# Kernel optimization log

Hardware: AMD Instinct MI355X
Metric: run time of the kernel (lower is better)

## Reference

```python
import jax, jax.numpy as jnp
import numpy as np

B, CIN, COUT, H, W = 4, 4, 8, 256, 256
FFTH, FFTW = 2 * H - 1, 2 * W - 1  # fftsize = insize + outsize - 1 (padding=True, stride=1)


def setup_inputs() -> dict:
    key = jax.random.key(0)
    k_im, k_w, k_b = jax.random.split(key, 3)
    im = jax.random.normal(k_im, (B, CIN, H, W), dtype=jnp.float32)
    # learned frequency-domain kernel, last dim = (real, imag)
    weight = jax.random.normal(k_w, (COUT, CIN, FFTH, FFTW, 2), dtype=jnp.float32)
    bias = jax.random.normal(k_b, (COUT, 1, 1), dtype=jnp.float32)
    return {"im": im, "weight": weight, "bias": bias}


def reference(im, weight, bias):
    b, cin, h, w = im.shape
    ffth, fftw = 2 * h - 1, 2 * w - 1
    # zero-pad spatially to fftsize; imaginary part is zero (torch pads a trailing complex dim)
    im_p = jnp.pad(im, ((0, 0), (0, 0), (0, ffth - h), (0, fftw - w)))
    f_im = jnp.fft.fft2(im_p.astype(jnp.complex64))              # [B, Cin, fftH, fftW]
    wc = jax.lax.complex(weight[..., 0], weight[..., 1])         # [O, Cin, fftH, fftW]
    # broadcast complex multiply + in-channel reduction fused as a per-frequency contraction;
    # ifft is linear so summing over in-channels before ifft matches the original math
    feats = jnp.einsum('bchw,ochw->bohw', f_im, wc)              # [B, O, fftH, fftW]
    real = jnp.fft.ifft2(feats).real                             # real_feats_mode='index' -> real part
    # crop: cropsize = fftsize - insize = (H-1, W-1); left = floor/2, right = ceil/2
    cl_h, cr_h = (h - 1) // 2, h // 2
    cl_w, cr_w = (w - 1) // 2, w // 2
    real = real[:, :, cl_h:ffth - cr_h, cl_w:fftw - cr_w]        # [B, O, H, W]
    return real + bias                                           # bias [O,1,1] broadcasts
```

## Files before the change

kernel.cpp:

```cpp
#include <hip/hip_runtime.h>
#include <math.h>

#define NN 511
#define HH 256
#define BB 4
#define CINC 4
#define COUTC 8
#define CROP 127
#define INV_NN2 (1.0f / ((float)NN * (float)NN))

typedef _Float16 f16;
typedef _Float16 f16x8 __attribute__((ext_vector_type(8)));
typedef float    f32x4 __attribute__((ext_vector_type(4)));

__device__ __forceinline__ void twid(int a, int b, float& c, float& s) {
    int m = (int)(((long long)a * (long long)b) % NN);
    float phi = (float)(2.0 * M_PI / (double)NN) * (float)m;
    __sincosf(phi, &s, &c);
}

__global__ void prep_Aa(f16* __restrict__ Aa) {
    int idx = blockIdx.x * 256 + threadIdx.x;
    int m = idx >> 8, y = idx & 255;
    float c, s;
    if (m < 256) { twid(m, y, c, s);      Aa[idx] = (f16)c;    }
    else         { twid(m - 256, y, c, s); Aa[idx] = (f16)(-s); }
}
__global__ void prep_Bb(f16* __restrict__ Bb) {
    int idx = blockIdx.x * 256 + threadIdx.x;
    int n = idx >> 9, k = idx & 511;
    float v = 0.f;
    if (n < 2 * NN) {
        int vv = (n < NN) ? n : n - NN;
        int x  = k & 255;
        float c, s; twid(vv, x, c, s);
        if (n < NN) v = (k < 256) ? c : s;
        else        v = (k < 256) ? -s : c;
    }
    Bb[idx] = (f16)v;
}
__global__ void prep_Bd(f16* __restrict__ Bd) {
    int idx = blockIdx.x * 256 + threadIdx.x;
    int n = idx >> 10, k = idx & 1023;
    float v = 0.f;
    if (k < 2 * NN) {
        int x  = n & 255;
        int vv = (k < NN) ? k : k - NN;
        float c, s; twid(vv, x + CROP, c, s);
        if (n < 256) v = (k < NN) ? c : -s;
        else         v = (k < NN) ? s : c;
    }
    Bd[idx] = (f16)v;
}
__global__ void prep_Ae(f16* __restrict__ Ae) {
    int idx = blockIdx.x * 256 + threadIdx.x;
    int y = idx >> 9, k = idx & 511;
    float c, s;
    if (k < 256) { twid(k, y + CROP, c, s);       Ae[idx] = (f16)c;    }
    else         { twid(k - 256, y + CROP, c, s); Ae[idx] = (f16)(-s); }
}
__global__ void prep_imT(const float* __restrict__ im, f16* __restrict__ imT) {
    int idx = blockIdx.x * 256 + threadIdx.x;
    int bc = idx >> 16, r = idx & 65535;
    int y = r >> 8, x = r & 255;
    imT[(size_t)bc * 65536 + x * 256 + y] = (f16)im[idx];
}
__global__ void zero_pad1024(f16* __restrict__ buf, int rows) {
    int r = blockIdx.x * 256 + threadIdx.x;
    if (r < rows) {
        buf[(size_t)r * 1024 + 1022] = (f16)0.f;
        buf[(size_t)r * 1024 + 1023] = (f16)0.f;
    }
}

__global__ void cmul_h(const f16* __restrict__ F, const float2* __restrict__ W,
                       f16* __restrict__ feats) {
    int idx = blockIdx.x * 256 + threadIdx.x;
    if (idx >= 256 * NN) return;
    int u = idx / NN, v = idx - u * NN;
    int u2 = (u == 0) ? 0 : NN - u;
    int v2 = (v == 0) ? 0 : NN - v;
    float fr[BB][CINC], fi[BB][CINC];
    #pragma unroll
    for (int b = 0; b < BB; ++b)
        #pragma unroll
        for (int c = 0; c < CINC; ++c) {
            size_t row = ((size_t)((b * CINC + c) * 256 + u)) * 1024;
            fr[b][c] = (float)F[row + v];
            fi[b][c] = (float)F[row + NN + v];
        }
    #pragma unroll
    for (int o = 0; o < COUTC; ++o) {
        float whr[CINC], whi[CINC];
        #pragma unroll
        for (int c = 0; c < CINC; ++c) {
            size_t base = (size_t)(o * CINC + c) * NN;
            float2 w1 = W[(base + u)  * NN + v];
            float2 w2 = W[(base + u2) * NN + v2];
            whr[c] = 0.5f * (w1.x + w2.x);
            whi[c] = 0.5f * (w1.y - w2.y);
        }
        #pragma unroll
        for (int b = 0; b < BB; ++b) {
            float hr = 0.f, hi = 0.f;
            #pragma unroll
            for (int c = 0; c < CINC; ++c) {
                hr += fr[b][c] * whr[c] - fi[b][c] * whi[c];
                hi += fr[b][c] * whi[c] + fi[b][c] * whr[c];
            }
            size_t orow = ((size_t)((b * COUTC + o) * 256 + u)) * 1024;
            feats[orow + v]      = (f16)hr;
            feats[orow + NN + v] = (f16)hi;
        }
    }
}

#define GLB_PTR(p) ((const __attribute__((address_space(1))) unsigned int*)(p))
#define LDS_PTR(p) ((__attribute__((address_space(3))) unsigned int*)(p))
__device__ __forceinline__ void gld16(const f16* g, f16* l) {
    __builtin_amdgcn_global_load_lds(GLB_PTR(g), LDS_PTR(l), 16, 0, 0);
}

template<int EPI>
__global__ __launch_bounds__(256)
void gemm128x64(const f16* __restrict__ A, const f16* __restrict__ Bt,
                f16* __restrict__ Ch, float* __restrict__ Cf,
                const float* __restrict__ bias,
                int Kt, int ldA, int ldB, size_t sA, size_t sB) {
    __shared__ __align__(16) f16 As[128 * 32];
    __shared__ __align__(16) f16 Bs[64 * 32];

    const int z  = blockIdx.z;
    const int m0 = blockIdx.x * 128;
    const int n0 = blockIdx.y * 64;
    A  += (size_t)z * sA;
    Bt += (size_t)z * sB;

    const int t  = threadIdx.x;
    const int r4 = t >> 2;
    const int c8 = (t & 3) << 3;
    const f16* Ap = A  + (size_t)(m0 + r4) * ldA + c8;
    const f16* Bp = Bt + (size_t)(n0 + r4) * ldB + c8;
    f16* lA = As + t * 8;
    f16* lB = Bs + t * 8;

    const int lane = t & 63, w = t >> 6;
    const int wm = (w >> 1) * 64, wn = (w & 1) * 32;
    const int col = lane & 15, quad = lane >> 4;
    const f16* a_base = As + (wm + col) * 32 + quad * 8;
    const f16* b_base = Bs + (wn + col) * 32 + quad * 8;

    f32x4 acc[4][2] = {};

    for (int kb = 0; kb < Kt; ++kb) {
        __syncthreads();
        gld16(Ap,            lA);
        gld16(Ap + 64 * ldA, lA + 2048);
        gld16(Bp,            lB);
        Ap += 32; Bp += 32;
        __syncthreads();
        f16x8 af[4], bf[2];
        #pragma unroll
        for (int i = 0; i < 4; ++i) af[i] = *(const f16x8*)(a_base + i * 16 * 32);
        #pragma unroll
        for (int j = 0; j < 2; ++j) bf[j] = *(const f16x8*)(b_base + j * 16 * 32);
        #pragma unroll
        for (int i = 0; i < 4; ++i)
            #pragma unroll
            for (int j = 0; j < 2; ++j)
                acc[i][j] = __builtin_amdgcn_mfma_f32_16x16x32_f16(af[i], bf[j], acc[i][j], 0, 0, 0);
    }

    #pragma unroll
    for (int i = 0; i < 4; ++i)
    #pragma unroll
    for (int j = 0; j < 2; ++j) {
        const int mbase = m0 + wm + i * 16 + quad * 4;
        const int ncol  = n0 + wn + j * 16 + col;
        #pragma unroll
        for (int r = 0; r < 4; ++r) {
            const int mm = mbase + r;
            const float val = acc[i][j][r];
            if constexpr (EPI == 0) {
                int u = mm & 255;
                int slot = (mm < 256) ? ncol : 256 + ncol;
                Ch[((size_t)(z * 256 + u)) * 512 + slot] = (f16)val;
            } else if constexpr (EPI == 1) {
                Ch[(size_t)mm * 1024 + ncol] = (f16)val;
            } else if constexpr (EPI == 2) {
                int bo = mm >> 8, u = mm & 255;
                int x    = (ncol < 256) ? ncol : ncol - 256;
                int slot = (ncol < 256) ? u : 256 + u;
                float sc = (u == 0) ? INV_NN2 : 2.f * INV_NN2;
                Ch[((size_t)((bo << 8) + x)) * 512 + slot] = (f16)(val * sc);
            } else {
                int bo = ncol >> 8, x = ncol & 255;
                Cf[((size_t)bo * 256 + mm) * 256 + x] = val + bias[bo & 7];
            }
        }
    }
}

extern "C" void kernel_launch(void* const* d_in, const int* in_sizes, int n_in,
                              void* d_out, int out_size, void* d_ws, size_t ws_size,
                              hipStream_t stream) {
    const float*  im   = (const float*)d_in[0];
    const float2* W    = (const float2*)d_in[1];
    const float*  bias = (const float*)d_in[2];
    float*        out  = (float*)d_out;

    char* ws = (char*)d_ws;
    f16* Aa    = (f16*)(ws);
    f16* Bb    = (f16*)(ws + 262144);
    f16* Bd    = (f16*)(ws + 1310720);
    f16* Ae    = (f16*)(ws + 2359296);
    f16* imT   = (f16*)(ws + 2621440);
    f16* T1    = (f16*)(ws + 4718592);
    f16* F     = (f16*)(ws + 8912896);
    f16* feats = (f16*)(ws + 17301504);
    f16* T2t   = (f16*)(ws + 34078720);

    prep_Aa <<<512,  256, 0, stream>>>(Aa);
    prep_Bb <<<2048, 256, 0, stream>>>(Bb);
    prep_Bd <<<2048, 256, 0, stream>>>(Bd);
    prep_Ae <<<512,  256, 0, stream>>>(Ae);
    prep_imT<<<4096, 256, 0, stream>>>(im, imT);
    zero_pad1024<<<32, 256, 0, stream>>>(feats, 8192);

    gemm128x64<0><<<dim3(4, 4, 16), 256, 0, stream>>>(Aa, imT, T1, nullptr, nullptr,
                                                      8, 256, 256, 0, 65536);
    gemm128x64<1><<<dim3(32, 16, 1), 256, 0, stream>>>(T1, Bb, F, nullptr, nullptr,
                                                       16, 512, 512, 0, 0);
    cmul_h<<<(256 * NN + 255) / 256, 256, 0, stream>>>(F, W, feats);
    gemm128x64<2><<<dim3(64, 8, 1), 256, 0, stream>>>(feats, Bd, T2t, nullptr, nullptr,
                                                      32, 1024, 1024, 0, 0);
    gemm128x64<3><<<dim3(2, 128, 1), 256, 0, stream>>>(Ae, T2t, nullptr, out, bias,
                                                       16, 512, 512, 0, 0);
}
```

Before: 181.9 us.

## Fuse prep kernels and double GEMM K-tile with XOR-swizzled LDS layout

New measurement: 170.6 us. -6.2%, faster.

```diff
diff --git a/kernel.cpp b/kernel.cpp
--- a/kernel.cpp
+++ b/kernel.cpp
@@ -14,62 +14,59 @@
 typedef float    f32x4 __attribute__((ext_vector_type(4)));
 
 __device__ __forceinline__ void twid(int a, int b, float& c, float& s) {
-    int m = (int)(((long long)a * (long long)b) % NN);
+    int m = (a * b) % NN;
     float phi = (float)(2.0 * M_PI / (double)NN) * (float)m;
     __sincosf(phi, &s, &c);
 }
 
-__global__ void prep_Aa(f16* __restrict__ Aa) {
+__global__ void prep_all(const float* __restrict__ im,
+                         f16* __restrict__ Aa, f16* __restrict__ Bb,
+                         f16* __restrict__ Bd, f16* __restrict__ Ae,
+                         f16* __restrict__ imT, f16* __restrict__ feats) {
     int idx = blockIdx.x * 256 + threadIdx.x;
-    int m = idx >> 8, y = idx & 255;
-    float c, s;
-    if (m < 256) { twid(m, y, c, s);      Aa[idx] = (f16)c;    }
-    else         { twid(m - 256, y, c, s); Aa[idx] = (f16)(-s); }
-}
-__global__ void prep_Bb(f16* __restrict__ Bb) {
-    int idx = blockIdx.x * 256 + threadIdx.x;
-    int n = idx >> 9, k = idx & 511;
-    float v = 0.f;
-    if (n < 2 * NN) {
-        int vv = (n < NN) ? n : n - NN;
-        int x  = k & 255;
-        float c, s; twid(vv, x, c, s);
-        if (n < NN) v = (k < 256) ? c : s;
-        else        v = (k < 256) ? -s : c;
-    }
-    Bb[idx] = (f16)v;
-}
-__global__ void prep_Bd(f16* __restrict__ Bd) {
-    int idx = blockIdx.x * 256 + threadIdx.x;
-    int n = idx >> 10, k = idx & 1023;
-    float v = 0.f;
-    if (k < 2 * NN) {
-        int x  = n & 255;
-        int vv = (k < NN) ? k : k - NN;
-        float c, s; twid(vv, x + CROP, c, s);
-        if (n < 256) v = (k < NN) ? c : -s;
-        else         v = (k < NN) ? s : c;
-    }
-    Bd[idx] = (f16)v;
-}
-__global__ void prep_Ae(f16* __restrict__ Ae) {
-    int idx = blockIdx.x * 256 + threadIdx.x;
-    int y = idx >> 9, k = idx & 511;
-    float c, s;
-    if (k < 256) { twid(k, y + CROP, c, s);       Ae[idx] = (f16)c;    }
-    else         { twid(k - 256, y + CROP, c, s); Ae[idx] = (f16)(-s); }
-}
-__global__ void prep_imT(const float* __restrict__ im, f16* __restrict__ imT) {
-    int idx = blockIdx.x * 256 + threadIdx.x;
-    int bc = idx >> 16, r = idx & 65535;
-    int y = r >> 8, x = r & 255;
-    imT[(size_t)bc * 65536 + x * 256 + y] = (f16)im[idx];
-}
-__global__ void zero_pad1024(f16* __restrict__ buf, int rows) {
-    int r = blockIdx.x * 256 + threadIdx.x;
-    if (r < rows) {
-        buf[(size_t)r * 1024 + 1022] = (f16)0.f;
-        buf[(size_t)r * 1024 + 1023] = (f16)0.f;
+    if (idx < 131072) {
+        int m = idx >> 8, y = idx & 255;
+        float c, s;
+        if (m < 256) { twid(m, y, c, s);       Aa[idx] = (f16)c;    }
+        else         { twid(m - 256, y, c, s); Aa[idx] = (f16)(-s); }
+    } else if (idx < 655360) {
+        int i = idx - 131072;
+        int n = i >> 9, k = i & 511;
+        float v = 0.f;
+        if (n < 2 * NN) {
+            int vv = (n < NN) ? n : n - NN;
+            int x  = k & 255;
+            float c, s; twid(vv, x, c, s);
+            if (n < NN) v = (k < 256) ? c : s;
+            else        v = (k < 256) ? -s : c;
+        }
+        Bb[i] = (f16)v;
+    } else if (idx < 1179648) {
+        int i = idx - 655360;
+        int n = i >> 10, k = i & 1023;
+        float v = 0.f;
+        if (k < 2 * NN) {
+            int x  = n & 255;
+            int vv = (k < NN) ? k : k - NN;
+            float c, s; twid(vv, x + CROP, c, s);
+            if (n < 256) v = (k < NN) ? c : -s;
+            else         v = (k < NN) ? s : c;
+        }
+        Bd[i] = (f16)v;
+    } else if (idx < 1310720) {
+        int i = idx - 1179648;
+        int y = i >> 9, k = i & 511;
+        float c, s;
+        if (k < 256) { twid(k, y + CROP, c, s);       Ae[i] = (f16)c;    }
+        else         { twid(k - 256, y + CROP, c, s); Ae[i] = (f16)(-s); }
+    } else if (idx < 2359296) {
+        int i = idx - 1310720;
+        int bc = i >> 16, r = i & 65535;
+        int y = r >> 8, x = r & 255;
+        imT[(size_t)bc * 65536 + x * 256 + y] = (f16)im[i];
+    } else if (idx < 2375680) {
+        int i = idx - 2359296;
+        feats[(size_t)(i >> 1) * 1024 + 1022 + (i & 1)] = (f16)0.f;
     }
 }
 
@@ -127,8 +124,8 @@
                 f16* __restrict__ Ch, float* __restrict__ Cf,
                 const float* __restrict__ bias,
                 int Kt, int ldA, int ldB, size_t sA, size_t sB) {
-    __shared__ __align__(16) f16 As[128 * 32];
-    __shared__ __align__(16) f16 Bs[64 * 32];
+    __shared__ __align__(16) f16 As[128 * 64];
+    __shared__ __align__(16) f16 Bs[64 * 64];
 
     const int z  = blockIdx.z;
     const int m0 = blockIdx.x * 128;
@@ -136,39 +133,55 @@
     A  += (size_t)z * sA;
     Bt += (size_t)z * sB;
 
-    const int t  = threadIdx.x;
-    const int r4 = t >> 2;
-    const int c8 = (t & 3) << 3;
-    const f16* Ap = A  + (size_t)(m0 + r4) * ldA + c8;
-    const f16* Bp = Bt + (size_t)(n0 + r4) * ldB + c8;
+    const int t    = threadIdx.x;
+    const int row  = t >> 3;
+    const int slot = t & 7;
+    const int kg   = (slot ^ (row & 7)) << 3;
+    const f16* Ap = A  + (size_t)(m0 + row) * ldA + kg;
+    const f16* Bp = Bt + (size_t)(n0 + row) * ldB + kg;
     f16* lA = As + t * 8;
     f16* lB = Bs + t * 8;
 
     const int lane = t & 63, w = t >> 6;
     const int wm = (w >> 1) * 64, wn = (w & 1) * 32;
     const int col = lane & 15, quad = lane >> 4;
-    const f16* a_base = As + (wm + col) * 32 + quad * 8;
-    const f16* b_base = Bs + (wn + col) * 32 + quad * 8;
+    const int aswz = col & 7;
+    const int offK0 = ((quad)     ^ aswz) << 3;
+    const int offK1 = ((4 + quad) ^ aswz) << 3;
+    const f16* a_col = As + (wm + col) * 64;
+    const f16* b_col = Bs + (wn + col) * 64;
 
     f32x4 acc[4][2] = {};
 
     for (int kb = 0; kb < Kt; ++kb) {
         __syncthreads();
-        gld16(Ap,            lA);
-        gld16(Ap + 64 * ldA, lA + 2048);
-        gld16(Bp,            lB);
-        Ap += 32; Bp += 32;
+        gld16(Ap,             lA);
+        gld16(Ap +  32 * ldA, lA + 2048);
+        gld16(Ap +  64 * ldA, lA + 4096);
+        gld16(Ap +  96 * ldA, lA + 6144);
+        gld16(Bp,             lB);
+        gld16(Bp +  32 * ldB, lB + 2048);
+        Ap += 64; Bp += 64;
         __syncthreads();
-        f16x8 af[4], bf[2];
-        #pragma unroll
-        for (int i = 0; i < 4; ++i) af[i] = *(const f16x8*)(a_base + i * 16 * 32);
-        #pragma unroll
-        for (int j = 0; j < 2; ++j) bf[j] = *(const f16x8*)(b_base + j * 16 * 32);
-        #pragma unroll
-        for (int i = 0; i < 4; ++i)
+        f16x8 af[4][2], bf[2][2];
+        #pragma unroll
+        for (int i = 0; i < 4; ++i) {
+            af[i][0] = *(const f16x8*)(a_col + i * 16 * 64 + offK0);
+            af[i][1] = *(const f16x8*)(a_col + i * 16 * 64 + offK1);
+        }
+        #pragma unroll
+        for (int j = 0; j < 2; ++j) {
+            bf[j][0] = *(const f16x8*)(b_col + j * 16 * 64 + offK0);
+            bf[j][1] = *(const f16x8*)(b_col + j * 16 * 64 + offK1);
+        }
+        #pragma unroll
+        for (int kk = 0; kk < 2; ++kk)
             #pragma unroll
-            for (int j = 0; j < 2; ++j)
-                acc[i][j] = __builtin_amdgcn_mfma_f32_16x16x32_f16(af[i], bf[j], acc[i][j], 0, 0, 0);
+            for (int i = 0; i < 4; ++i)
+                #pragma unroll
+                for (int j = 0; j < 2; ++j)
+                    acc[i][j] = __builtin_amdgcn_mfma_f32_16x16x32_f16(
+                        af[i][kk], bf[j][kk], acc[i][j], 0, 0, 0);
     }
 
     #pragma unroll
@@ -183,16 +196,16 @@
             const float val = acc[i][j][r];
             if constexpr (EPI == 0) {
                 int u = mm & 255;
-                int slot = (mm < 256) ? ncol : 256 + ncol;
-                Ch[((size_t)(z * 256 + u)) * 512 + slot] = (f16)val;
+                int slotc = (mm < 256) ? ncol : 256 + ncol;
+                Ch[((size_t)(z * 256 + u)) * 512 + slotc] = (f16)val;
             } else if constexpr (EPI == 1) {
                 Ch[(size_t)mm * 1024 + ncol] = (f16)val;
             } else if constexpr (EPI == 2) {
                 int bo = mm >> 8, u = mm & 255;
-                int x    = (ncol < 256) ? ncol : ncol - 256;
-                int slot = (ncol < 256) ? u : 256 + u;
+                int x     = (ncol < 256) ? ncol : ncol - 256;
+                int slotc = (ncol < 256) ? u : 256 + u;
                 float sc = (u == 0) ? INV_NN2 : 2.f * INV_NN2;
-                Ch[((size_t)((bo << 8) + x)) * 512 + slot] = (f16)(val * sc);
+                Ch[((size_t)((bo << 8) + x)) * 512 + slotc] = (f16)(val * sc);
             } else {
                 int bo = ncol >> 8, x = ncol & 255;
                 Cf[((size_t)bo * 256 + mm) * 256 + x] = val + bias[bo & 7];
@@ -220,20 +233,15 @@
     f16* feats = (f16*)(ws + 17301504);
     f16* T2t   = (f16*)(ws + 34078720);
 
-    prep_Aa <<<512,  256, 0, stream>>>(Aa);
-    prep_Bb <<<2048, 256, 0, stream>>>(Bb);
-    prep_Bd <<<2048, 256, 0, stream>>>(Bd);
-    prep_Ae <<<512,  256, 0, stream>>>(Ae);
-    prep_imT<<<4096, 256, 0, stream>>>(im, imT);
-    zero_pad1024<<<32, 256, 0, stream>>>(feats, 8192);
+    prep_all<<<9280, 256, 0, stream>>>(im, Aa, Bb, Bd, Ae, imT, feats);
 
     gemm128x64<0><<<dim3(4, 4, 16), 256, 0, stream>>>(Aa, imT, T1, nullptr, nullptr,
-                                                      8, 256, 256, 0, 65536);
+                                                      4, 256, 256, 0, 65536);
     gemm128x64<1><<<dim3(32, 16, 1), 256, 0, stream>>>(T1, Bb, F, nullptr, nullptr,
-                                                       16, 512, 512, 0, 0);
+                                                       8, 512, 512, 0, 0);
     cmul_h<<<(256 * NN + 255) / 256, 256, 0, stream>>>(F, W, feats);
     gemm128x64<2><<<dim3(64, 8, 1), 256, 0, stream>>>(feats, Bd, T2t, nullptr, nullptr,
-                                                      32, 1024, 1024, 0, 0);
+                                                      16, 1024, 1024, 0, 0);
     gemm128x64<3><<<dim3(2, 128, 1), 256, 0, stream>>>(Ae, T2t, nullptr, out, bias,
-                                                       16, 512, 512, 0, 0);
-}
+                                                       8, 512, 512, 0, 0);
+}
```
